# Kernel optimization log

Hardware: AMD Instinct MI355X
Metric: run time of the kernel (lower is better)

The kernel has to match this reference:

```python
import jax, jax.numpy as jnp
import numpy as np

NUM_EMBEDDINGS = 512
EMBEDDING_DIM = 64
COMMITMENT_COST = 0.25


def setup_inputs() -> dict:
    key = jax.random.key(0)
    k1, k2 = jax.random.split(key)
    z_e = jax.random.normal(k1, (16, EMBEDDING_DIM, 64, 64), dtype=jnp.float32)
    # embedding.weight initialized uniform(-1/K, 1/K) in the torch module
    lim = 1.0 / NUM_EMBEDDINGS
    embedding = jax.random.uniform(
        k2, (NUM_EMBEDDINGS, EMBEDDING_DIM), dtype=jnp.float32,
        minval=-lim, maxval=lim)
    return {"z_e": z_e, "embedding": embedding}


def reference(z_e, embedding):
    b, c, h, w = z_e.shape
    K = embedding.shape[0]
    # NCHW -> NHWC -> [N, D]
    flat = jnp.transpose(z_e, (0, 2, 3, 1)).reshape(-1, c)  # [N, D]
    distances = (jnp.sum(flat * flat, axis=1, keepdims=True)
                 + jnp.sum(embedding * embedding, axis=1)
                 - 2.0 * jnp.matmul(flat, embedding.T))
    encoding_indices = jnp.argmin(distances, axis=1)  # [N]
    # one_hot @ embedding == gather (same math, avoids materializing [N,K] fp mm)
    z_q_flat = jnp.take(embedding, encoding_indices, axis=0)  # [N, D]
    z_q = jnp.transpose(z_q_flat.reshape(b, h, w, c), (0, 3, 1, 2))  # NCHW
    # EMA codebook: only commitment loss, codes updated via EMA (detached)
    e_latent_loss = jnp.mean((jax.lax.stop_gradient(z_q) - z_e) ** 2)
    loss = COMMITMENT_COST * e_latent_loss
    # straight-through estimator
    z_q_st = z_e + jax.lax.stop_gradient(z_q - z_e)
    # perplexity from one-hot assignment frequencies
    counts = jnp.zeros((K,), dtype=jnp.float32).at[encoding_indices].add(1.0)
    avg_probs = counts / flat.shape[0]
    perplexity = jnp.exp(-jnp.sum(avg_probs * jnp.log(avg_probs + 1e-10)))
    return z_q_st, loss, perplexity, encoding_indices
```

## Files before the change

### kernel.cpp

```cpp
#include <hip/hip_runtime.h>

#define BATCH 16
#define CH 64
#define HW 4096
#define NPIX 65536
#define KCODES 512
#define DDIM 64
#define NELEM 4194304

#define OUT_LOSS 4194304
#define OUT_PPL  4194305
#define OUT_IDX  4194306

#define MARGIN 2.2e-4f

typedef short bf16x8 __attribute__((ext_vector_type(8)));
typedef float f32x4  __attribute__((ext_vector_type(4)));

__device__ __forceinline__ float rnd(float s) {
    asm volatile("" : "+v"(s));
    return s;
}
__device__ __forceinline__ short f2bf(float f) {
    unsigned u = __builtin_bit_cast(unsigned, f);
    unsigned r = (u + 0x7fffu + ((u >> 16) & 1u)) >> 16;
    return (short)r;
}

__global__ void k_prep(const float* __restrict__ emb, float* __restrict__ e2,
                       bf16x8* __restrict__ Bh, float4* __restrict__ P4) {
    int gid = blockIdx.x * 256 + threadIdx.x;
    if (gid < 4096) {
        int tn = gid >> 7, rem = gid & 127;
        int chunk = (rem >> 6) & 1, q = (rem >> 4) & 3, i = rem & 15;
        int code = tn * 16 + i;
        const float* src = emb + code * DDIM + chunk * 32 + q * 8;
        bf16x8 h;
        #pragma unroll
        for (int j = 0; j < 8; ++j) h[j] = f2bf(src[j]);
        Bh[gid] = h;
    } else if (gid < 4608) {
        int k = gid - 4096;
        const float* row = emb + k * DDIM;
        float r[8];
        #pragma unroll
        for (int j = 0; j < 8; ++j) { float v = row[j]; r[j] = rnd(v * v); }
        #pragma unroll
        for (int m = 1; m < 8; ++m)
            #pragma unroll
            for (int j = 0; j < 8; ++j) { float v = row[8 * m + j]; r[j] += rnd(v * v); }
        e2[k] = ((r[0] + r[1]) + (r[2] + r[3])) + ((r[4] + r[5]) + (r[6] + r[7]));
    } else if (gid < 12800) {
        int pid = gid - 4608;
        int kk = pid >> 10, c4 = (pid >> 6) & 15, lane = pid & 63;
        int code = lane * 8 + kk;
        P4[pid] = *(const float4*)(emb + code * DDIM + c4 * 4);
    }
}

__global__ __launch_bounds__(512, 4) void k_dist(
        const float* __restrict__ z_e, const float* __restrict__ emb,
        const bf16x8* __restrict__ Bh, const float* __restrict__ e2g,
        int* __restrict__ idx, int* __restrict__ glist, int* __restrict__ nflag,
        int* __restrict__ counts, float* __restrict__ slots,
        float* __restrict__ out) {
    __shared__ bf16x8 Bs[4096];
    __shared__ float e2s[512];
    __shared__ int   hist[512];
    __shared__ int   flist[128];
    __shared__ int   fcnt, fbase;

    int t = threadIdx.x;
    int pxbase = blockIdx.x * 128;
    int batch = pxbase >> 12;
    int p0 = pxbase & 4095;
    const float* zb = z_e + (size_t)batch * (CH * HW) + p0;

    bf16x8 rb[8];
    #pragma unroll
    for (int i = 0; i < 8; ++i) rb[i] = Bh[i * 512 + t];

    hist[t] = 0;
    e2s[t] = e2g[t];
    if (t == 0) fcnt = 0;

    int w = t >> 6, lane = t & 63, col = lane & 15, quad = lane >> 4;
    int px = w * 16 + col;

    bf16x8 a0, a1;
    #pragma unroll
    for (int j = 0; j < 8; ++j) {
        a0[j] = f2bf(zb[(quad * 8 + j) * HW + px]);
        a1[j] = f2bf(zb[(32 + quad * 8 + j) * HW + px]);
    }

    #pragma unroll
    for (int i = 0; i < 8; ++i) Bs[i * 512 + t] = rb[i];
    __syncthreads();

    float m1[4], m2[4];
    int   i1[4];
    #pragma unroll
    for (int r = 0; r < 4; ++r) { m1[r] = 1e30f; m2[r] = 1e30f; i1[r] = 0; }

    #pragma unroll 4
    for (int tn = 0; tn < 32; ++tn) {
        bf16x8 c0 = Bs[tn * 128 + lane];
        bf16x8 c1 = Bs[tn * 128 + 64 + lane];
        float e2v = e2s[tn * 16 + col];
        int n = tn * 16 + col;
        f32x4 acc = {0.f, 0.f, 0.f, 0.f};
        acc = __builtin_amdgcn_mfma_f32_16x16x32_bf16(a0, c0, acc, 0, 0, 0);
        acc = __builtin_amdgcn_mfma_f32_16x16x32_bf16(a1, c1, acc, 0, 0, 0);
        #pragma unroll
        for (int r = 0; r < 4; ++r) {
            float d = fmaf(-2.0f, acc[r], e2v);
            if (d < m1[r])      { m2[r] = m1[r]; m1[r] = d; i1[r] = n; }
            else if (d < m2[r]) { m2[r] = d; }
        }
    }

    #pragma unroll
    for (int off = 1; off < 16; off <<= 1) {
        #pragma unroll
        for (int r = 0; r < 4; ++r) {
            float om1 = __shfl_xor(m1[r], off);
            float om2 = __shfl_xor(m2[r], off);
            int   oi  = __shfl_xor(i1[r], off);
            if (om1 < m1[r] || (om1 == m1[r] && oi < i1[r])) {
                m2[r] = fminf(m1[r], om2);
                m1[r] = om1;
                i1[r] = oi;
            } else {
                m2[r] = fminf(m2[r], om1);
            }
        }
    }

    if (col == 0) {
        #pragma unroll
        for (int r = 0; r < 4; ++r) {
            int g = pxbase + w * 16 + quad * 4 + r;
            idx[g] = i1[r];
            out[OUT_IDX + g] = (float)i1[r];
            atomicAdd(&hist[i1[r]], 1);
            if (m2[r] - m1[r] < MARGIN) {
                int pos = atomicAdd(&fcnt, 1);
                flist[pos] = g;
            }
        }
    }

    int q4 = lane & 3;
    int bidx[4];
    #pragma unroll
    for (int j = 0; j < 4; ++j) bidx[j] = __shfl(i1[j], q4 << 4);
    const float* zw = zb + w * 16;
    float* ow = out + (size_t)batch * (CH * HW) + p0 + w * 16;
    float lsum = 0.0f;
    #pragma unroll
    for (int it = 0; it < 4; ++it) {
        int c = it * 16 + (lane >> 2);
        float4 ze = *(const float4*)(zw + c * HW + q4 * 4);
        float d0 = emb[bidx[0] * DDIM + c] - ze.x;
        float d1 = emb[bidx[1] * DDIM + c] - ze.y;
        float d2 = emb[bidx[2] * DDIM + c] - ze.z;
        float d3 = emb[bidx[3] * DDIM + c] - ze.w;
        float4 o = {ze.x + d0, ze.y + d1, ze.z + d2, ze.w + d3};
        *(float4*)(ow + c * HW + q4 * 4) = o;
        lsum = lsum + d0 * d0 + d1 * d1 + d2 * d2 + d3 * d3;
    }
    #pragma unroll
    for (int off = 32; off; off >>= 1) lsum += __shfl_down(lsum, off);
    if (lane == 0) atomicAdd(&slots[((blockIdx.x * 8 + w) & 63) * 16], lsum);

    __syncthreads();
    int v0 = hist[t];
    if (v0) atomicAdd(&counts[t], v0);
    if (t == 0) fbase = atomicAdd(nflag, fcnt);
    __syncthreads();
    if (t < fcnt) glist[fbase + t] = flist[t];
}

__global__ __launch_bounds__(256) void k_refine(
        const float* __restrict__ z_e, const float* __restrict__ emb,
        const float* __restrict__ e2, const float4* __restrict__ P4,
        const int* __restrict__ glist, const int* __restrict__ nflag,
        int* __restrict__ idx, int* __restrict__ counts,
        float* __restrict__ slots, float* __restrict__ out) {
    __shared__ float4 Ps[8192];
    __shared__ float  xs[4][64];

    int t = threadIdx.x;
    int w = t >> 6, lane = t & 63;
    int n = nflag[0];
    if (blockIdx.x >= n) return;

    #pragma unroll
    for (int i = 0; i < 32; ++i) Ps[i * 256 + t] = P4[i * 256 + t];
    __syncthreads();

    float4 ea = ((const float4*)e2)[lane * 2];
    float4 eb = ((const float4*)e2)[lane * 2 + 1];
    float e2v[8] = {ea.x, ea.y, ea.z, ea.w, eb.x, eb.y, eb.z, eb.w};

    int wid = blockIdx.x * 4 + w;
    for (int j = wid; j < n; j += 1024) {
        int g = glist[j];
        int b = g >> 12, p = g & 4095;
        xs[w][lane] = z_e[(size_t)b * (CH * HW) + (size_t)lane * HW + p];
        __threadfence_block();

        const float* xr = xs[w];
        float r[8];
        #pragma unroll
        for (int jj = 0; jj < 8; ++jj) { float v = xr[jj]; r[jj] = rnd(v * v); }
        #pragma unroll
        for (int mm = 1; mm < 8; ++mm)
            #pragma unroll
            for (int jj = 0; jj < 8; ++jj) { float v = xr[8 * mm + jj]; r[jj] += rnd(v * v); }
        float x2 = ((r[0] + r[1]) + (r[2] + r[3])) + ((r[4] + r[5]) + (r[6] + r[7]));

        float bestd = INFINITY;
        int besti = 1 << 30;
        #pragma unroll
        for (int kk = 0; kk < 8; ++kk) {
            double d0 = 0.0, d1 = 0.0, d2 = 0.0, d3 = 0.0;
            #pragma unroll
            for (int c4 = 0; c4 < 16; ++c4) {
                float4 xq = *(const float4*)&xr[c4 * 4];
                float4 ev = Ps[(kk * 16 + c4) * 64 + lane];
                d0 = fma((double)xq.x, (double)ev.x, d0);
                d1 = fma((double)xq.y, (double)ev.y, d1);
                d2 = fma((double)xq.z, (double)ev.z, d2);
                d3 = fma((double)xq.w, (double)ev.w, d3);
            }
            float dotf = (float)((d0 + d1) + (d2 + d3));
            float tt = x2 + e2v[kk];
            float d = tt - 2.0f * dotf;
            if (d < bestd) { bestd = d; besti = lane * 8 + kk; }
        }
        #pragma unroll
        for (int off = 32; off; off >>= 1) {
            float od = __shfl_down(bestd, off);
            int   oi = __shfl_down(besti, off);
            if (od < bestd || (od == bestd && oi < besti)) { bestd = od; besti = oi; }
        }
        besti = __shfl(besti, 0);

        int old = idx[g];
        if (besti != old) {
            float xc = xr[lane];
            float qn = emb[besti * DDIM + lane];
            float qo = emb[old * DDIM + lane];
            float dn = qn - xc, dold = qo - xc;
            out[(size_t)b * (CH * HW) + (size_t)lane * HW + p] = xc + dn;
            float delta = dn * dn - dold * dold;
            #pragma unroll
            for (int off = 32; off; off >>= 1) delta += __shfl_down(delta, off);
            if (lane == 0) {
                atomicAdd(&slots[(wid & 63) * 16], delta);
                atomicAdd(&counts[old], -1);
                atomicAdd(&counts[besti], 1);
                idx[g] = besti;
                out[OUT_IDX + g] = (float)besti;
            }
        }
    }
}

__global__ void k_final(const int* __restrict__ counts,
                        const float* __restrict__ slots,
                        float* __restrict__ out) {
    int t = threadIdx.x;
    float cnt = (float)counts[t];
    float pb = cnt * (1.0f / 65536.0f);
    float term = pb * logf(pb + 1e-10f);
    #pragma unroll
    for (int off = 32; off; off >>= 1) term += __shfl_down(term, off);
    __shared__ float ls[8];
    __shared__ float lsum;
    int lane = t & 63, w = t >> 6;
    if (lane == 0) ls[w] = term;
    if (w == 0) {
        float s2 = slots[lane * 16];
        #pragma unroll
        for (int off = 32; off; off >>= 1) s2 += __shfl_down(s2, off);
        if (lane == 0) lsum = s2;
    }
    __syncthreads();
    if (t == 0) {
        float s = 0.0f;
        #pragma unroll
        for (int i = 0; i < 8; ++i) s += ls[i];
        out[OUT_PPL]  = expf(-s);
        out[OUT_LOSS] = 0.25f * (lsum / (float)NELEM);
    }
}

extern "C" void kernel_launch(void* const* d_in, const int* in_sizes, int n_in,
                              void* d_out, int out_size, void* d_ws, size_t ws_size,
                              hipStream_t stream) {
    const float* z_e = (const float*)d_in[0];
    const float* emb = (const float*)d_in[1];
    float* out = (float*)d_out;
    char* ws = (char*)d_ws;

    int*    idx    = (int*)(ws);
    int*    glist  = (int*)(ws + 262144);
    float*  e2     = (float*)(ws + 524288);
    int*    nflag  = (int*)(ws + 526336);
    int*    counts = (int*)(ws + 526400);
    float*  slots  = (float*)(ws + 528448);
    bf16x8* Bh     = (bf16x8*)(ws + 532544);
    float4* P4     = (float4*)(ws + 598080);

    hipMemsetAsync(ws + 526336, 0, 532544 - 526336, stream);

    k_prep<<<50, 256, 0, stream>>>(emb, e2, Bh, P4);
    k_dist<<<NPIX / 128, 512, 0, stream>>>(z_e, emb, Bh, e2, idx, glist, nflag, counts, slots, out);
    k_refine<<<256, 256, 0, stream>>>(z_e, emb, e2, P4, glist, nflag, idx, counts, slots, out);
    k_final<<<1, 512, 0, stream>>>(counts, slots, out);
}
```

Measured before the change: 139.6 us.

## Fuse near-tie FP64 refinement into distance kernel, drop separate refine pass

Rescores flagged near-tie pixels inside k_dist with an exact double-precision dot product, where each thread handles one code and reads a transposed fp32 codebook. Final indices are then resolved before the z_q/loss write, so the k_refine launch, the global flag list and the index scratch buffer all go away. This removes a kernel launch, a 128KB shared codebook load per refine block, and the corrective second writes to the output. The cost is extra syncs and FP64 work inside the main kernel, which stalls blocks that contain flagged pixels.

```diff
diff --git a/kernel.cpp b/kernel.cpp
--- a/kernel.cpp
+++ b/kernel.cpp
@@ -28,7 +28,7 @@
 }
 
 __global__ void k_prep(const float* __restrict__ emb, float* __restrict__ e2,
-                       bf16x8* __restrict__ Bh, float4* __restrict__ P4) {
+                       bf16x8* __restrict__ Bh, float4* __restrict__ ET4) {
     int gid = blockIdx.x * 256 + threadIdx.x;
     if (gid < 4096) {
         int tn = gid >> 7, rem = gid & 127;
@@ -52,23 +52,31 @@
         e2[k] = ((r[0] + r[1]) + (r[2] + r[3])) + ((r[4] + r[5]) + (r[6] + r[7]));
     } else if (gid < 12800) {
         int pid = gid - 4608;
-        int kk = pid >> 10, c4 = (pid >> 6) & 15, lane = pid & 63;
-        int code = lane * 8 + kk;
-        P4[pid] = *(const float4*)(emb + code * DDIM + c4 * 4);
+        int c = pid >> 7, kg = pid & 127;
+        float4 v;
+        v.x = emb[(kg * 4 + 0) * DDIM + c];
+        v.y = emb[(kg * 4 + 1) * DDIM + c];
+        v.z = emb[(kg * 4 + 2) * DDIM + c];
+        v.w = emb[(kg * 4 + 3) * DDIM + c];
+        ET4[c * 128 + kg] = v;
     }
 }
 
 __global__ __launch_bounds__(512, 4) void k_dist(
         const float* __restrict__ z_e, const float* __restrict__ emb,
         const bf16x8* __restrict__ Bh, const float* __restrict__ e2g,
-        int* __restrict__ idx, int* __restrict__ glist, int* __restrict__ nflag,
+        const float* __restrict__ ET,
         int* __restrict__ counts, float* __restrict__ slots,
         float* __restrict__ out) {
     __shared__ bf16x8 Bs[4096];
     __shared__ float e2s[512];
     __shared__ int   hist[512];
+    __shared__ int   best_px[128];
     __shared__ int   flist[128];
-    __shared__ int   fcnt, fbase;
+    __shared__ float xflag[16][64];
+    __shared__ float wd[16][8];
+    __shared__ int   wi[16][8];
+    __shared__ int   fcnt;
 
     int t = threadIdx.x;
     int pxbase = blockIdx.x * 128;
@@ -140,21 +148,79 @@
     if (col == 0) {
         #pragma unroll
         for (int r = 0; r < 4; ++r) {
-            int g = pxbase + w * 16 + quad * 4 + r;
-            idx[g] = i1[r];
-            out[OUT_IDX + g] = (float)i1[r];
-            atomicAdd(&hist[i1[r]], 1);
+            int lp = w * 16 + quad * 4 + r;
+            best_px[lp] = i1[r];
             if (m2[r] - m1[r] < MARGIN) {
                 int pos = atomicAdd(&fcnt, 1);
-                flist[pos] = g;
-            }
-        }
+                flist[pos] = lp;
+            }
+        }
+    }
+    __syncthreads();
+
+    int nf = fcnt;
+    for (int base = 0; base < nf; base += 16) {
+        int nc = min(16, nf - base);
+        for (int i = t; i < nc * 64; i += 512) {
+            int f = i >> 6, c = i & 63;
+            xflag[f][c] = zb[c * HW + flist[base + f]];
+        }
+        __syncthreads();
+        for (int f = 0; f < nc; ++f) {
+            const float* xr = xflag[f];
+            float r[8];
+            #pragma unroll
+            for (int jj = 0; jj < 8; ++jj) { float v = xr[jj]; r[jj] = rnd(v * v); }
+            #pragma unroll
+            for (int mm = 1; mm < 8; ++mm)
+                #pragma unroll
+                for (int jj = 0; jj < 8; ++jj) { float v = xr[8 * mm + jj]; r[jj] += rnd(v * v); }
+            float x2 = ((r[0] + r[1]) + (r[2] + r[3])) + ((r[4] + r[5]) + (r[6] + r[7]));
+
+            double d0 = 0.0, d1 = 0.0, d2 = 0.0, d3 = 0.0;
+            #pragma unroll
+            for (int c4 = 0; c4 < 16; ++c4) {
+                float4 xq = *(const float4*)&xr[c4 * 4];
+                d0 = fma((double)xq.x, (double)ET[(c4 * 4 + 0) * 512 + t], d0);
+                d1 = fma((double)xq.y, (double)ET[(c4 * 4 + 1) * 512 + t], d1);
+                d2 = fma((double)xq.z, (double)ET[(c4 * 4 + 2) * 512 + t], d2);
+                d3 = fma((double)xq.w, (double)ET[(c4 * 4 + 3) * 512 + t], d3);
+            }
+            float dotf = (float)((d0 + d1) + (d2 + d3));
+            float tt = x2 + e2s[t];
+            float d = tt - 2.0f * dotf;
+            float bd = d; int bi = t;
+            #pragma unroll
+            for (int off = 32; off; off >>= 1) {
+                float od = __shfl_down(bd, off);
+                int   oi = __shfl_down(bi, off);
+                if (od < bd || (od == bd && oi < bi)) { bd = od; bi = oi; }
+            }
+            if (lane == 0) { wd[f][w] = bd; wi[f][w] = bi; }
+        }
+        __syncthreads();
+        if (t < nc) {
+            float bd = wd[t][0]; int bi = wi[t][0];
+            #pragma unroll
+            for (int ww = 1; ww < 8; ++ww) {
+                float od = wd[t][ww]; int oi = wi[t][ww];
+                if (od < bd || (od == bd && oi < bi)) { bd = od; bi = oi; }
+            }
+            best_px[flist[base + t]] = bi;
+        }
+        __syncthreads();
+    }
+
+    if (t < 128) {
+        int bi = best_px[t];
+        out[OUT_IDX + pxbase + t] = (float)bi;
+        atomicAdd(&hist[bi], 1);
     }
 
     int q4 = lane & 3;
     int bidx[4];
     #pragma unroll
-    for (int j = 0; j < 4; ++j) bidx[j] = __shfl(i1[j], q4 << 4);
+    for (int j = 0; j < 4; ++j) bidx[j] = best_px[w * 16 + q4 * 4 + j];
     const float* zw = zb + w * 16;
     float* ow = out + (size_t)batch * (CH * HW) + p0 + w * 16;
     float lsum = 0.0f;
@@ -177,96 +243,6 @@
     __syncthreads();
     int v0 = hist[t];
     if (v0) atomicAdd(&counts[t], v0);
-    if (t == 0) fbase = atomicAdd(nflag, fcnt);
-    __syncthreads();
-    if (t < fcnt) glist[fbase + t] = flist[t];
-}
-
-__global__ __launch_bounds__(256) void k_refine(
-        const float* __restrict__ z_e, const float* __restrict__ emb,
-        const float* __restrict__ e2, const float4* __restrict__ P4,
-        const int* __restrict__ glist, const int* __restrict__ nflag,
-        int* __restrict__ idx, int* __restrict__ counts,
-        float* __restrict__ slots, float* __restrict__ out) {
-    __shared__ float4 Ps[8192];
-    __shared__ float  xs[4][64];
-
-    int t = threadIdx.x;
-    int w = t >> 6, lane = t & 63;
-    int n = nflag[0];
-    if (blockIdx.x >= n) return;
-
-    #pragma unroll
-    for (int i = 0; i < 32; ++i) Ps[i * 256 + t] = P4[i * 256 + t];
-    __syncthreads();
-
-    float4 ea = ((const float4*)e2)[lane * 2];
-    float4 eb = ((const float4*)e2)[lane * 2 + 1];
-    float e2v[8] = {ea.x, ea.y, ea.z, ea.w, eb.x, eb.y, eb.z, eb.w};
-
-    int wid = blockIdx.x * 4 + w;
-    for (int j = wid; j < n; j += 1024) {
-        int g = glist[j];
-        int b = g >> 12, p = g & 4095;
-        xs[w][lane] = z_e[(size_t)b * (CH * HW) + (size_t)lane * HW + p];
-        __threadfence_block();
-
-        const float* xr = xs[w];
-        float r[8];
-        #pragma unroll
-        for (int jj = 0; jj < 8; ++jj) { float v = xr[jj]; r[jj] = rnd(v * v); }
-        #pragma unroll
-        for (int mm = 1; mm < 8; ++mm)
-            #pragma unroll
-            for (int jj = 0; jj < 8; ++jj) { float v = xr[8 * mm + jj]; r[jj] += rnd(v * v); }
-        float x2 = ((r[0] + r[1]) + (r[2] + r[3])) + ((r[4] + r[5]) + (r[6] + r[7]));
-
-        float bestd = INFINITY;
-        int besti = 1 << 30;
-        #pragma unroll
-        for (int kk = 0; kk < 8; ++kk) {
-            double d0 = 0.0, d1 = 0.0, d2 = 0.0, d3 = 0.0;
-            #pragma unroll
-            for (int c4 = 0; c4 < 16; ++c4) {
-                float4 xq = *(const float4*)&xr[c4 * 4];
-                float4 ev = Ps[(kk * 16 + c4) * 64 + lane];
-                d0 = fma((double)xq.x, (double)ev.x, d0);
-                d1 = fma((double)xq.y, (double)ev.y, d1);
-                d2 = fma((double)xq.z, (double)ev.z, d2);
-                d3 = fma((double)xq.w, (double)ev.w, d3);
-            }
-            float dotf = (float)((d0 + d1) + (d2 + d3));
-            float tt = x2 + e2v[kk];
-            float d = tt - 2.0f * dotf;
-            if (d < bestd) { bestd = d; besti = lane * 8 + kk; }
-        }
-        #pragma unroll
-        for (int off = 32; off; off >>= 1) {
-            float od = __shfl_down(bestd, off);
-            int   oi = __shfl_down(besti, off);
-            if (od < bestd || (od == bestd && oi < besti)) { bestd = od; besti = oi; }
-        }
-        besti = __shfl(besti, 0);
-
-        int old = idx[g];
-        if (besti != old) {
-            float xc = xr[lane];
-            float qn = emb[besti * DDIM + lane];
-            float qo = emb[old * DDIM + lane];
-            float dn = qn - xc, dold = qo - xc;
-            out[(size_t)b * (CH * HW) + (size_t)lane * HW + p] = xc + dn;
-            float delta = dn * dn - dold * dold;
-            #pragma unroll
-            for (int off = 32; off; off >>= 1) delta += __shfl_down(delta, off);
-            if (lane == 0) {
-                atomicAdd(&slots[(wid & 63) * 16], delta);
-                atomicAdd(&counts[old], -1);
-                atomicAdd(&counts[besti], 1);
-                idx[g] = besti;
-                out[OUT_IDX + g] = (float)besti;
-            }
-        }
-    }
 }
 
 __global__ void k_final(const int* __restrict__ counts,
@@ -306,19 +282,15 @@
     float* out = (float*)d_out;
     char* ws = (char*)d_ws;
 
-    int*    idx    = (int*)(ws);
-    int*    glist  = (int*)(ws + 262144);
-    float*  e2     = (float*)(ws + 524288);
-    int*    nflag  = (int*)(ws + 526336);
-    int*    counts = (int*)(ws + 526400);
-    float*  slots  = (float*)(ws + 528448);
-    bf16x8* Bh     = (bf16x8*)(ws + 532544);
-    float4* P4     = (float4*)(ws + 598080);
-
-    hipMemsetAsync(ws + 526336, 0, 532544 - 526336, stream);
-
-    k_prep<<<50, 256, 0, stream>>>(emb, e2, Bh, P4);
-    k_dist<<<NPIX / 128, 512, 0, stream>>>(z_e, emb, Bh, e2, idx, glist, nflag, counts, slots, out);
-    k_refine<<<256, 256, 0, stream>>>(z_e, emb, e2, P4, glist, nflag, idx, counts, slots, out);
+    float*  e2     = (float*)(ws);
+    int*    counts = (int*)(ws + 2048);
+    float*  slots  = (float*)(ws + 4096);
+    bf16x8* Bh     = (bf16x8*)(ws + 8192);
+    float*  ET     = (float*)(ws + 73728);
+
+    hipMemsetAsync(ws + 2048, 0, 8192 - 2048, stream);
+
+    k_prep<<<50, 256, 0, stream>>>(emb, e2, Bh, (float4*)ET);
+    k_dist<<<NPIX / 128, 512, 0, stream>>>(z_e, emb, Bh, e2, ET, counts, slots, out);
     k_final<<<1, 512, 0, stream>>>(counts, slots, out);
 }
```

Result: slower. 418.2 us (+199.6%).
